# Optimization experiments

Hardware: AMD Instinct MI355X
Metric: run time of the kernel (lower is better)

## Reference

```python
import jax, jax.numpy as jnp
import numpy as np

NUM_HEAVY = 1024
N_ITERS = 50
FETCH_K_RATIO = 9.0 / 8.0
EPS = 1.0


def rmsnorm(x, gamma):
    scale = gamma.shape[0] ** 0.5
    normed = x / jnp.maximum(jnp.linalg.norm(x, axis=-1, keepdims=True), 1e-12)
    return normed * scale * gamma


def feedforward(x, gamma, w1, b1, w2, b2):
    h = rmsnorm(x, gamma)
    h = jax.nn.gelu(h @ w1.T + b1, approximate=False)
    return h @ w2.T + b2


def coor_descent(s, n_iters, k, eps):
    # s: [b, n] router logits; faithful to lucidrains coor_descent (no mask, const eps)
    logk = jnp.log(jnp.asarray(k, s.dtype))
    a0 = jnp.zeros_like(s[..., :1])
    b0 = -s

    def body(carry, _):
        a, b = carry
        a = eps * (logk - jax.nn.logsumexp((s + b) / eps, axis=-1, keepdims=True))
        b = -jax.nn.relu(s + a)
        return (a, b), None

    (a, b), _ = jax.lax.scan(body, (a0, b0), None, length=n_iters)
    return jnp.exp((s + a + b) / eps)


def setup_inputs() -> dict:
    key = jax.random.key(0)
    ks = jax.random.split(key, 12)
    b, n, dim = 8, 8192, 1024
    d_light, d_heavy = int(dim * 0.5), dim * 4

    def lin(k, dout, din):
        bound = 1.0 / np.sqrt(din)
        k1, k2 = jax.random.split(k)
        w = jax.random.uniform(k1, (dout, din), jnp.float32, -bound, bound)
        bb = jax.random.uniform(k2, (dout,), jnp.float32, -bound, bound)
        return w, bb

    x = jax.random.normal(ks[0], (b, n, dim), jnp.float32)
    routing_token = jax.random.normal(ks[1], (dim,), jnp.float32)
    w1_l, b1_l = lin(ks[2], d_light, dim)
    w2_l, b2_l = lin(ks[3], dim, d_light)
    w1_h, b1_h = lin(ks[4], d_heavy, dim)
    w2_h, b2_h = lin(ks[5], dim, d_heavy)
    return dict(
        x=x, routing_token=routing_token,
        gamma_l=jnp.ones((dim,), jnp.float32), w1_l=w1_l, b1_l=b1_l, w2_l=w2_l, b2_l=b2_l,
        gamma_h=jnp.ones((dim,), jnp.float32), w1_h=w1_h, b1_h=b1_h, w2_h=w2_h, b2_h=b2_h,
    )


def reference(x, routing_token, gamma_l, w1_l, b1_l, w2_l, b2_l,
              gamma_h, w1_h, b1_h, w2_h, b2_h):
    b, n, dim = x.shape
    # light branch on all tokens
    light_out = feedforward(x, gamma_l, w1_l, b1_l, w2_l, b2_l)

    # router (coor_descent, num_routing_tokens=1, no mask)
    s = jnp.einsum('bnd,d->bn', x, routing_token)
    effective_k = min(NUM_HEAVY * FETCH_K_RATIO, n)
    scores = coor_descent(s, N_ITERS, effective_k, EPS)
    selected_scores, selected_indices = jax.lax.top_k(scores, NUM_HEAVY)
    # straight-through: value -> 1, grad flows through selected_scores
    selected_scores = selected_scores + jax.lax.stop_gradient(1.0 - selected_scores)

    # gather -> heavy FFN -> scale -> scatter back
    routed = jnp.take_along_axis(x, selected_indices[..., None], axis=1)  # [b, k, d]
    routed_out = feedforward(routed, gamma_h, w1_h, b1_h, w2_h, b2_h)
    routed_out = routed_out * selected_scores[..., None]

    batch_range = jnp.arange(b)[:, None]
    heavy_out = jnp.zeros_like(x).at[batch_range, selected_indices].set(routed_out)
    return light_out + heavy_out
```

## Files before the change

kernel.cpp:

```cpp
#include <hip/hip_runtime.h>
#include <cstdint>
#include <cstddef>


#define DEV __device__ __forceinline__

typedef __bf16 bf16x8 __attribute__((ext_vector_type(8)));
typedef float floatx4 __attribute__((ext_vector_type(4)));

DEV unsigned short f2bf(float f) {
  unsigned int u = __float_as_uint(f);
  u += 0x7FFFu + ((u >> 16) & 1u);
  return (unsigned short)(u >> 16);
}

__global__ __launch_bounds__(256) void convw_gamma_kernel(
    const float* __restrict__ w, const float* __restrict__ gamma,
    unsigned short* __restrict__ wb, int n) {
  int i = blockIdx.x * 256 + threadIdx.x;
  if (i < n) wb[i] = f2bf(w[i] * gamma[i & 1023]);
}
__global__ __launch_bounds__(256) void convw_kernel(
    const float* __restrict__ w, unsigned short* __restrict__ wb, int n) {
  int i = blockIdx.x * 256 + threadIdx.x;
  if (i < n) wb[i] = f2bf(w[i]);
}

__global__ __launch_bounds__(256) void prep_kernel(
    const float* __restrict__ x, const float* __restrict__ rt,
    unsigned short* __restrict__ xn, double* __restrict__ s) {
  const int token = blockIdx.x;
  const int tid = threadIdx.x;
  const float4 v = ((const float4*)(x + (size_t)token * 1024))[tid];
  const float4 r = ((const float4*)rt)[tid];
  float ss = v.x * v.x + v.y * v.y + v.z * v.z + v.w * v.w;
  double dot = (double)v.x * r.x + (double)v.y * r.y + (double)v.z * r.z + (double)v.w * r.w;
  const int wave = tid >> 6, lane = tid & 63;
#pragma unroll
  for (int off = 32; off; off >>= 1) {
    ss += __shfl_down(ss, off);
    dot += __shfl_down(dot, off);
  }
  __shared__ float ssr[4];
  __shared__ double dr[4];
  __shared__ float scale_sh;
  if (lane == 0) { ssr[wave] = ss; dr[wave] = dot; }
  __syncthreads();
  if (tid == 0) {
    float tot = ssr[0] + ssr[1] + ssr[2] + ssr[3];
    scale_sh = 32.0f / fmaxf(sqrtf(tot), 1e-12f);
    s[token] = dr[0] + dr[1] + dr[2] + dr[3];
  }
  __syncthreads();
  const float sc = scale_sh;
  ushort4 o;
  o.x = f2bf(v.x * sc); o.y = f2bf(v.y * sc);
  o.z = f2bf(v.z * sc); o.w = f2bf(v.w * sc);
  ((ushort4*)(xn + (size_t)token * 1024))[tid] = o;
}

__global__ __launch_bounds__(1024) void coor_kernel(
    const double* __restrict__ s, double* __restrict__ a_out) {
  const int b = blockIdx.x, tid = threadIdx.x;
  const int wave = tid >> 6, lane = tid & 63;
  __shared__ double red[16];
  __shared__ double bcast;
  const double* sb = s + (size_t)b * 8192;
  double sv[8], es[8];
#pragma unroll
  for (int i = 0; i < 8; ++i) {
    sv[i] = sb[tid * 8 + i];
    es[i] = exp(sv[i]);
  }
  const double logk = log(1152.0);
  double a = logk - log(8192.0);
  for (int it = 0; it < 49; ++it) {
    const double th = -a;
    const double eth = exp(th);
    double sum = 0.0;
#pragma unroll
    for (int i = 0; i < 8; ++i) sum += (sv[i] < th) ? es[i] : eth;
#pragma unroll
    for (int off = 32; off; off >>= 1) sum += __shfl_down(sum, off);
    if (lane == 0) red[wave] = sum;
    __syncthreads();
    if (tid == 0) {
      double t = 0.0;
      for (int i = 0; i < 16; ++i) t += red[i];
      bcast = logk - log(t);
    }
    __syncthreads();
    a = bcast;
  }
  if (tid == 0) a_out[b] = a;
}

__global__ __launch_bounds__(1024) void select_kernel(
    const double* __restrict__ s, const double* __restrict__ a_in,
    int* __restrict__ sel, int* __restrict__ invsel) {
  const int b = blockIdx.x, tid = threadIdx.x;
  const int wave = tid >> 6, lane = tid & 63;
  const double a = a_in[b];
  const double* sb = s + (size_t)b * 8192;
  const int base = tid * 8;
  double sv[8];
  bool ind[8];
  int cnt = 0;
#pragma unroll
  for (int i = 0; i < 8; ++i) {
    sv[i] = sb[base + i];
    ind[i] = (sv[i] + a >= 0.0);
    cnt += ind[i] ? 1 : 0;
  }
  __shared__ int sc[1024];
  sc[tid] = cnt;
  __syncthreads();
  for (int off = 1; off < 1024; off <<= 1) {
    int v = sc[tid];
    int add = (tid >= off) ? sc[tid - off] : 0;
    __syncthreads();
    sc[tid] = v + add;
    __syncthreads();
  }
  const int m = sc[1023];
  int p = sc[tid] - cnt;
#pragma unroll
  for (int i = 0; i < 8; ++i) {
    int w = -1;
    if (ind[i]) {
      if (p < 1024) { sel[b * 1024 + p] = base + i; w = p; }
      ++p;
    }
    invsel[b * 8192 + base + i] = w;
  }
  if (m >= 1024) return;

  __shared__ double rv[16];
  __shared__ int ri[16];
  __shared__ int gsel;
  bool taken[8] = {false, false, false, false, false, false, false, false};
  const int need = 1024 - m;
  for (int t = 0; t < need; ++t) {
    double bvv = -1.0e300;
    int bi = 0x7FFFFFFF;
#pragma unroll
    for (int i = 0; i < 8; ++i)
      if (!ind[i] && !taken[i] && sv[i] > bvv) { bvv = sv[i]; bi = base + i; }
#pragma unroll
    for (int off = 32; off; off >>= 1) {
      double ov = __shfl_down(bvv, off);
      int oi = __shfl_down(bi, off);
      if (ov > bvv || (ov == bvv && oi < bi)) { bvv = ov; bi = oi; }
    }
    if (lane == 0) { rv[wave] = bvv; ri[wave] = bi; }
    __syncthreads();
    if (tid == 0) {
      double mv = rv[0]; int mi = ri[0];
      for (int i = 1; i < 16; ++i)
        if (rv[i] > mv || (rv[i] == mv && ri[i] < mi)) { mv = rv[i]; mi = ri[i]; }
      gsel = mi;
      sel[b * 1024 + m + t] = mi;
      invsel[b * 8192 + mi] = m + t;
    }
    __syncthreads();
    const int g = gsel;
    if (g >= base && g < base + 8) taken[g - base] = true;
    __syncthreads();
  }
}


enum {
  RA00 = 0,      RA01 = 16384,  RA10 = 32768,  RA11 = 49152,
  RB00 = 65536,  RB01 = 81920,  RB10 = 98304,  RB11 = 114688
};

#define VMCNT(n) asm volatile("s_waitcnt vmcnt(" #n ")" ::: "memory")
#define BARR() __builtin_amdgcn_s_barrier()
#define SCHED0() __builtin_amdgcn_sched_barrier(0)

#define STG_A(DST, KOFF)                                                      \
  do {                                                                        \
    _Pragma("unroll") for (int r_ = 0; r_ < 2; ++r_)                          \
        __builtin_amdgcn_global_load_lds(                                     \
            (__attribute__((address_space(1))) void*)(Asrc[r_] + (KOFF)),     \
            (__attribute__((address_space(3))) void*)(sh + (DST) + r_ * 8192 +\
                                                     ldsW),                   \
            16, 0, 0);                                                        \
  } while (0)

#define STG_B(DST, KOFF)                                                      \
  do {                                                                        \
    _Pragma("unroll") for (int r_ = 0; r_ < 2; ++r_)                          \
        __builtin_amdgcn_global_load_lds(                                     \
            (__attribute__((address_space(1))) void*)(Bsrc[r_] + (KOFF)),     \
            (__attribute__((address_space(3))) void*)(sh + (DST) + r_ * 8192 +\
                                                     ldsW),                   \
            16, 0, 0);                                                        \
  } while (0)

#define PH(RAOFF, RBOFF, MH, LOADB, STG)                                      \
  do {                                                                        \
    bf16x8 a_[4];                                                             \
    _Pragma("unroll") for (int f_ = 0; f_ < 4; ++f_) a_[f_] =                 \
        *(const bf16x8*)(sh + (RAOFF) + f_ * 2048 + rbA);                     \
    if (LOADB) {                                                              \
      _Pragma("unroll") for (int n_ = 0; n_ < 4; ++n_) bq[n_] =               \
          *(const bf16x8*)(sh + (RBOFF) + n_ * 2048 + rbB);                   \
    }                                                                         \
    STG;                                                                      \
    __builtin_amdgcn_s_setprio(1);                                            \
    _Pragma("unroll") for (int f_ = 0; f_ < 4; ++f_)                          \
        _Pragma("unroll") for (int n_ = 0; n_ < 4; ++n_) acc[(MH) + f_][n_] = \
            __builtin_amdgcn_mfma_f32_16x16x32_bf16(a_[f_], bq[n_],           \
                                                    acc[(MH) + f_][n_], 0, 0, \
                                                    0);                       \
    __builtin_amdgcn_s_setprio(0);                                            \
  } while (0)

#define ITER_FULL(I)                                                          \
  do {                                                                        \
    const int ks4 = ((2 * (I) + 1) << 6) + 32;                                \
    const int ks1 = ((2 * (I) + 2) << 6);                                     \
    const int ks2 = ks1 + 32;                                                 \
    const int ks3 = ((2 * (I) + 3) << 6);                                     \
    PH(RA00, RB00, 0, 1, STG_A(RA11, ks4));                                   \
    PH(RA00 + 8192, RB00, 4, 0, STG_B(RB11, ks4));                            \
    VMCNT(8); BARR(); SCHED0();                                               \
    PH(RA01, RB01, 0, 1, STG_A(RA00, ks1));                                   \
    PH(RA01 + 8192, RB01, 4, 0, STG_B(RB00, ks1));                            \
    VMCNT(8); BARR(); SCHED0();                                               \
    PH(RA10, RB10, 0, 1, STG_A(RA01, ks2));                                   \
    PH(RA10 + 8192, RB10, 4, 0, STG_B(RB01, ks2));                            \
    VMCNT(8); BARR(); SCHED0();                                               \
    PH(RA11, RB11, 0, 1, STG_A(RA10, ks3));                                   \
    PH(RA11 + 8192, RB11, 4, 0, STG_B(RB10, ks3));                            \
    VMCNT(8); BARR(); SCHED0();                                               \
  } while (0)

#define ITER_LAST(I)                                                          \
  do {                                                                        \
    const int ks4 = ((2 * (I) + 1) << 6) + 32;                                \
    PH(RA00, RB00, 0, 1, STG_A(RA11, ks4));                                   \
    PH(RA00 + 8192, RB00, 4, 0, STG_B(RB11, ks4));                            \
    VMCNT(8); BARR(); SCHED0();                                               \
    PH(RA01, RB01, 0, 1, );                                                   \
    PH(RA01 + 8192, RB01, 4, 0, );                                            \
    VMCNT(4); BARR(); SCHED0();                                               \
    PH(RA10, RB10, 0, 1, );                                                   \
    PH(RA10 + 8192, RB10, 4, 0, );                                            \
    VMCNT(0); BARR(); SCHED0();                                               \
    PH(RA11, RB11, 0, 1, );                                                   \
    PH(RA11 + 8192, RB11, 4, 0, );                                            \
  } while (0)

template <int MODE, bool SELA>
__global__ __launch_bounds__(512, 2) void gemm8p_kernel(
    const unsigned short* __restrict__ A, const unsigned short* __restrict__ B,
    const float* __restrict__ bias, float* __restrict__ outF,
    unsigned short* __restrict__ outH, const int* __restrict__ sel,
    const float* __restrict__ hA, const float* __restrict__ hB,
    float* __restrict__ outF2, int M, int N, int K) {
  __shared__ alignas(16) char sh[131072];

  const int tiles_n = N >> 8;
  const int nwg = gridDim.x;
  const int bid = blockIdx.x;
  const int cpx = nwg >> 3;
  const int swz = (bid & 7) * cpx + (bid >> 3);

  int tile = swz, ksplit = 0;
  if (MODE == 3) { ksplit = swz >= (nwg >> 1); tile = swz & ((nwg >> 1) - 1); }
  const int Kloop = (MODE == 3) ? (K >> 1) : K;
  const int kbase = (MODE == 3) ? ksplit * (K >> 1) : 0;
  const int bm = tile / tiles_n, bn = tile - bm * tiles_n;

  const int tid = threadIdx.x;
  const int wave = tid >> 6, lane = tid & 63;
  const int l16 = lane & 15, q = lane >> 4;
  const int wm = wave >> 2, wn = wave & 3;

  const int slA = (((wm * 4 + q) ^ (l16 & 7)) << 4);
  const int slB = ((((wn >> 1) * 4 + q) ^ (l16 & 7)) << 4);
  const int rbA = l16 * 128 + slA;
  const int rbB = (wn & 1) * 8192 + l16 * 128 + slB;

  const int ssrc = (tid & 7) ^ ((tid >> 3) & 7);
  const int hfold = ssrc >> 2, chunk = ssrc & 3;
  const unsigned short* Asrc[2];
  const unsigned short* Bsrc[2];
#pragma unroll
  for (int r = 0; r < 2; ++r) {
    const int growA = bm * 256 + r * 64 + (tid >> 3) + hfold * 128;
    const int growB = bn * 256 + r * 64 + (tid >> 3) + hfold * 128;
    if (SELA) {
      const int bb = growA >> 10;
      Asrc[r] = A + ((size_t)((bb << 13) + sel[growA])) * K + kbase + chunk * 8;
    } else {
      Asrc[r] = A + (size_t)growA * K + kbase + chunk * 8;
    }
    Bsrc[r] = B + (size_t)growB * K + kbase + chunk * 8;
  }
  const int ldsW = wave * 1024;

  floatx4 acc[8][4];
#pragma unroll
  for (int i = 0; i < 8; ++i)
#pragma unroll
    for (int j = 0; j < 4; ++j) acc[i][j] = 0.0f;
  bf16x8 bq[4];

  STG_A(RA00, 0);  STG_B(RB00, 0);
  STG_A(RA01, 32); STG_B(RB01, 32);
  STG_A(RA10, 64); STG_B(RB10, 64);
  VMCNT(8); BARR(); SCHED0();

  const int NI = Kloop >> 7;
#pragma unroll 1
  for (int i = 0; i < NI - 1; ++i) ITER_FULL(i);
  ITER_LAST(NI - 1);

  const int gm0 = bm * 256 + wm * 128 + q * 4;
  const int gn0 = bn * 256 + wn * 64 + l16;
  float* const oF = (MODE == 3 && ksplit) ? outF2 : outF;
#pragma unroll
  for (int m = 0; m < 8; ++m) {
#pragma unroll
    for (int n = 0; n < 4; ++n) {
      const int col = gn0 + n * 16;
      const float bv = (MODE == 3 && ksplit) ? 0.0f : bias[col];
#pragma unroll
      for (int r = 0; r < 4; ++r) {
        const int row = gm0 + m * 16 + r;
        float v = acc[m][n][r] + bv;
        if (MODE == 0) {
          float g = 0.5f * v * (1.0f + erff(v * 0.70710678118654752f));
          outH[(size_t)row * N + col] = f2bf(g);
        } else if (MODE == 2) {
          const int slot = sel[row];
          if (slot >= 0) {
            const size_t hrow = (((size_t)(row >> 13)) << 10) + slot;
            v += hA[(hrow << 10) + col] + hB[(hrow << 10) + col];
          }
          outF[(size_t)row * N + col] = v;
        } else {
          oF[(size_t)row * N + col] = v;
        }
      }
    }
  }
}

extern "C" void kernel_launch(void* const* d_in, const int* in_sizes, int n_in,
                              void* d_out, int out_size, void* d_ws, size_t ws_size,
                              hipStream_t stream) {
  const float* x    = (const float*)d_in[0];
  const float* rt   = (const float*)d_in[1];
  const float* g_l  = (const float*)d_in[2];
  const float* w1_l = (const float*)d_in[3];
  const float* b1_l = (const float*)d_in[4];
  const float* w2_l = (const float*)d_in[5];
  const float* b2_l = (const float*)d_in[6];
  const float* g_h  = (const float*)d_in[7];
  const float* w1_h = (const float*)d_in[8];
  const float* b1_h = (const float*)d_in[9];
  const float* w2_h = (const float*)d_in[10];
  const float* b2_h = (const float*)d_in[11];
  float* out = (float*)d_out;

  char* ws = (char*)d_ws;
  size_t off = 0;
  auto alloc = [&](size_t bytes) -> char* {
    char* p = ws + off;
    off += (bytes + 255) & ~(size_t)255;
    return p;
  };
  unsigned short* xn  = (unsigned short*)alloc((size_t)65536 * 1024 * 2);
  double* s           = (double*)alloc((size_t)65536 * 8);
  double* a_out       = (double*)alloc(256);
  int* sel            = (int*)alloc(8192 * 4);
  int* invsel         = (int*)alloc((size_t)65536 * 4);
  unsigned short* w1l = (unsigned short*)alloc((size_t)512 * 1024 * 2);
  unsigned short* w2l = (unsigned short*)alloc((size_t)1024 * 512 * 2);
  unsigned short* w1h = (unsigned short*)alloc((size_t)4096 * 1024 * 2);
  unsigned short* w2h = (unsigned short*)alloc((size_t)1024 * 4096 * 2);
  unsigned short* h1  = (unsigned short*)alloc((size_t)33554432 * 2);
  float* hA           = (float*)alloc((size_t)8192 * 1024 * 4);
  float* hB           = (float*)alloc((size_t)8192 * 1024 * 4);
  if (off > ws_size) return;

  convw_gamma_kernel<<<524288 / 256, 256, 0, stream>>>(w1_l, g_l, w1l, 524288);
  convw_kernel<<<524288 / 256, 256, 0, stream>>>(w2_l, w2l, 524288);
  convw_gamma_kernel<<<4194304 / 256, 256, 0, stream>>>(w1_h, g_h, w1h, 4194304);
  convw_kernel<<<4194304 / 256, 256, 0, stream>>>(w2_h, w2h, 4194304);

  prep_kernel<<<65536, 256, 0, stream>>>(x, rt, xn, s);
  coor_kernel<<<8, 1024, 0, stream>>>(s, a_out);
  select_kernel<<<8, 1024, 0, stream>>>(s, a_out, sel, invsel);

  gemm8p_kernel<0, true><<<512, 512, 0, stream>>>(
      xn, w1h, b1_h, nullptr, h1, sel, nullptr, nullptr, nullptr, 8192, 4096, 1024);
  gemm8p_kernel<3, false><<<256, 512, 0, stream>>>(
      h1, w2h, b2_h, hA, nullptr, nullptr, nullptr, nullptr, hB, 8192, 1024, 4096);
  gemm8p_kernel<0, false><<<512, 512, 0, stream>>>(
      xn, w1l, b1_l, nullptr, h1, nullptr, nullptr, nullptr, nullptr, 65536, 512, 1024);
  gemm8p_kernel<2, false><<<1024, 512, 0, stream>>>(
      h1, w2l, b2_l, out, nullptr, invsel, hA, hB, nullptr, 65536, 1024, 512);
}
```

Before: 1.017 ms.

## Unfuse heavy-branch scatter-add into a separate kernel and issue stage loads earlier

The per-element invsel lookup and gathered heavy-output add are removed from the final light GEMM epilogue. A separate kernel now adds hA+hB into the 8192 selected output rows after the light GEMM writes plain results. The invsel array and its writes in select_kernel go away, which makes the epilogue lighter and removes the inverse-index memory traffic. In exchange there is an extra kernel launch and a read-modify-write of 32MB of out rows. The GEMM phase macro also issues the global-to-LDS stage loads before the LDS fragment reads instead of after them.

```diff
diff --git a/kernel.cpp b/kernel.cpp
--- a/kernel.cpp
+++ b/kernel.cpp
@@ -97,7 +97,7 @@
 
 __global__ __launch_bounds__(1024) void select_kernel(
     const double* __restrict__ s, const double* __restrict__ a_in,
-    int* __restrict__ sel, int* __restrict__ invsel) {
+    int* __restrict__ sel) {
   const int b = blockIdx.x, tid = threadIdx.x;
   const int wave = tid >> 6, lane = tid & 63;
   const double a = a_in[b];
@@ -126,12 +126,10 @@
   int p = sc[tid] - cnt;
 #pragma unroll
   for (int i = 0; i < 8; ++i) {
-    int w = -1;
     if (ind[i]) {
-      if (p < 1024) { sel[b * 1024 + p] = base + i; w = p; }
+      if (p < 1024) sel[b * 1024 + p] = base + i;
       ++p;
     }
-    invsel[b * 8192 + base + i] = w;
   }
   if (m >= 1024) return;
 
@@ -160,13 +158,27 @@
         if (rv[i] > mv || (rv[i] == mv && ri[i] < mi)) { mv = rv[i]; mi = ri[i]; }
       gsel = mi;
       sel[b * 1024 + m + t] = mi;
-      invsel[b * 8192 + mi] = m + t;
     }
     __syncthreads();
     const int g = gsel;
     if (g >= base && g < base + 8) taken[g - base] = true;
     __syncthreads();
   }
+}
+
+__global__ __launch_bounds__(256) void heavy_add_kernel(
+    const float* __restrict__ hA, const float* __restrict__ hB,
+    const int* __restrict__ sel, float* __restrict__ out) {
+  const int r = blockIdx.x;
+  const int b = r >> 10;
+  const int idx = sel[r];
+  const size_t orow = ((size_t)(b << 13) + idx) << 10;
+  const size_t hrow = (size_t)r << 10;
+  float4 o = ((const float4*)(out + orow))[threadIdx.x];
+  const float4 a = ((const float4*)(hA + hrow))[threadIdx.x];
+  const float4 c = ((const float4*)(hB + hrow))[threadIdx.x];
+  o.x += a.x + c.x; o.y += a.y + c.y; o.z += a.z + c.z; o.w += a.w + c.w;
+  ((float4*)(out + orow))[threadIdx.x] = o;
 }
 
 
@@ -201,6 +213,7 @@
 
 #define PH(RAOFF, RBOFF, MH, LOADB, STG)                                      \
   do {                                                                        \
+    STG;                                                                      \
     bf16x8 a_[4];                                                             \
     _Pragma("unroll") for (int f_ = 0; f_ < 4; ++f_) a_[f_] =                 \
         *(const bf16x8*)(sh + (RAOFF) + f_ * 2048 + rbA);                     \
@@ -208,7 +221,6 @@
       _Pragma("unroll") for (int n_ = 0; n_ < 4; ++n_) bq[n_] =               \
           *(const bf16x8*)(sh + (RBOFF) + n_ * 2048 + rbB);                   \
     }                                                                         \
-    STG;                                                                      \
     __builtin_amdgcn_s_setprio(1);                                            \
     _Pragma("unroll") for (int f_ = 0; f_ < 4; ++f_)                          \
         _Pragma("unroll") for (int n_ = 0; n_ < 4; ++n_) acc[(MH) + f_][n_] = \
@@ -259,7 +271,6 @@
     const unsigned short* __restrict__ A, const unsigned short* __restrict__ B,
     const float* __restrict__ bias, float* __restrict__ outF,
     unsigned short* __restrict__ outH, const int* __restrict__ sel,
-    const float* __restrict__ hA, const float* __restrict__ hB,
     float* __restrict__ outF2, int M, int N, int K) {
   __shared__ alignas(16) char sh[131072];
 
@@ -336,13 +347,6 @@
         if (MODE == 0) {
           float g = 0.5f * v * (1.0f + erff(v * 0.70710678118654752f));
           outH[(size_t)row * N + col] = f2bf(g);
-        } else if (MODE == 2) {
-          const int slot = sel[row];
-          if (slot >= 0) {
-            const size_t hrow = (((size_t)(row >> 13)) << 10) + slot;
-            v += hA[(hrow << 10) + col] + hB[(hrow << 10) + col];
-          }
-          outF[(size_t)row * N + col] = v;
         } else {
           oF[(size_t)row * N + col] = v;
         }
@@ -379,7 +383,6 @@
   double* s           = (double*)alloc((size_t)65536 * 8);
   double* a_out       = (double*)alloc(256);
   int* sel            = (int*)alloc(8192 * 4);
-  int* invsel         = (int*)alloc((size_t)65536 * 4);
   unsigned short* w1l = (unsigned short*)alloc((size_t)512 * 1024 * 2);
   unsigned short* w2l = (unsigned short*)alloc((size_t)1024 * 512 * 2);
   unsigned short* w1h = (unsigned short*)alloc((size_t)4096 * 1024 * 2);
@@ -396,14 +399,15 @@
 
   prep_kernel<<<65536, 256, 0, stream>>>(x, rt, xn, s);
   coor_kernel<<<8, 1024, 0, stream>>>(s, a_out);
-  select_kernel<<<8, 1024, 0, stream>>>(s, a_out, sel, invsel);
+  select_kernel<<<8, 1024, 0, stream>>>(s, a_out, sel);
 
   gemm8p_kernel<0, true><<<512, 512, 0, stream>>>(
-      xn, w1h, b1_h, nullptr, h1, sel, nullptr, nullptr, nullptr, 8192, 4096, 1024);
+      xn, w1h, b1_h, nullptr, h1, sel, nullptr, 8192, 4096, 1024);
   gemm8p_kernel<3, false><<<256, 512, 0, stream>>>(
-      h1, w2h, b2_h, hA, nullptr, nullptr, nullptr, nullptr, hB, 8192, 1024, 4096);
+      h1, w2h, b2_h, hA, nullptr, nullptr, hB, 8192, 1024, 4096);
   gemm8p_kernel<0, false><<<512, 512, 0, stream>>>(
-      xn, w1l, b1_l, nullptr, h1, nullptr, nullptr, nullptr, nullptr, 65536, 512, 1024);
-  gemm8p_kernel<2, false><<<1024, 512, 0, stream>>>(
-      h1, w2l, b2_l, out, nullptr, invsel, hA, hB, nullptr, 65536, 1024, 512);
-}
+      xn, w1l, b1_l, nullptr, h1, nullptr, nullptr, 65536, 512, 1024);
+  gemm8p_kernel<1, false><<<1024, 512, 0, stream>>>(
+      h1, w2l, b2_l, out, nullptr, nullptr, nullptr, 65536, 1024, 512);
+  heavy_add_kernel<<<8192, 256, 0, stream>>>(hA, hB, sel, out);
+}
```

After: 933.5 us. 8.2% less time.
